# Kernel tuning notes

Hardware: AMD Instinct MI355X
Metric: run time of the kernel (lower is better)

Reference implementation:

```python
import jax, jax.numpy as jnp
import numpy as np

B, T, V, E, H = 512, 256, 50000, 512, 1024


def setup_inputs() -> dict:
    key = jax.random.key(0)
    ks = jax.random.split(key, 10)
    s_in = 1.0 / np.sqrt(E + H)  # torch Linear default init scale
    s_fc = 1.0 / np.sqrt(H)
    return {
        "x": jax.random.randint(ks[0], (B, T), 0, V),
        "emb": jax.random.normal(ks[1], (V, E), dtype=jnp.float32),
        "W_r": jax.random.uniform(ks[2], (E + H, H), jnp.float32, -s_in, s_in),
        "b_r": jax.random.uniform(ks[3], (H,), jnp.float32, -s_in, s_in),
        "W_z": jax.random.uniform(ks[4], (E + H, H), jnp.float32, -s_in, s_in),
        "b_z": jax.random.uniform(ks[5], (H,), jnp.float32, -s_in, s_in),
        "W_c": jax.random.uniform(ks[6], (E + H, H), jnp.float32, -s_in, s_in),
        "b_c": jax.random.uniform(ks[7], (H,), jnp.float32, -s_in, s_in),
        "W_fc": jax.random.uniform(ks[8], (H, 1), jnp.float32, -s_fc, s_fc),
        "b_fc": jax.random.uniform(ks[9], (1,), jnp.float32, -s_fc, s_fc),
    }


def reference(x, emb, W_r, b_r, W_z, b_z, W_c, b_c, W_fc, b_fc):
    embedded = emb[x]                      # [B, T, E]
    xs = jnp.swapaxes(embedded, 0, 1)      # [T, B, E] for scan over time
    h0 = jnp.zeros((x.shape[0], H), dtype=emb.dtype)

    # fuse r and z gates: same input, one GEMM
    W_rz = jnp.concatenate([W_r, W_z], axis=1)   # [E+H, 2H]
    b_rz = jnp.concatenate([b_r, b_z], axis=0)   # [2H]

    def step(h, xt):
        combined = jnp.concatenate([xt, h], axis=1)          # [B, E+H]
        rz = jax.nn.sigmoid(combined @ W_rz + b_rz)          # [B, 2H]
        r, z = rz[:, :H], rz[:, H:]
        cc = jnp.concatenate([xt, r * h], axis=1)            # [B, E+H]
        h_tilde = jnp.tanh(cc @ W_c + b_c)                   # [B, H]
        h_new = (1.0 - z) * h + z * h_tilde
        return h_new, None

    h_T, _ = jax.lax.scan(step, h0, xs)
    return jax.nn.sigmoid(h_T @ W_fc + b_fc)                 # [B, 1]
```

## Files before the change

kernel.cpp:

```cpp
#include <hip/hip_runtime.h>
#include <hip/hip_bf16.h>

#define B_ 512
#define T_ 256
#define E_ 512
#define H_ 1024
#define K_ 1536

typedef __attribute__((ext_vector_type(4))) float f32x4;
typedef __attribute__((ext_vector_type(8))) short s16x8;
typedef __attribute__((ext_vector_type(4))) unsigned int u32x4;
typedef __attribute__((ext_vector_type(2))) unsigned int u32x2;

typedef unsigned int u32_g __attribute__((address_space(1)));
typedef unsigned int u32_l __attribute__((address_space(3)));

static __device__ __forceinline__ void gload16(const void* g, void* l) {
    __builtin_amdgcn_global_load_lds((const u32_g*)g, (u32_l*)l, 16, 0, 0);
}

static __device__ __forceinline__ short f2b(float f) {
    union { float f; unsigned u; } v; v.f = f;
    unsigned r = v.u + 0x7FFFu + ((v.u >> 16) & 1u);
    return (short)(r >> 16);
}
static __device__ __forceinline__ float bf2f(short s) {
    union { unsigned u; float f; } v; v.u = ((unsigned)(unsigned short)s) << 16;
    return v.f;
}
static __device__ __forceinline__ float sigmoidf_(float v) {
    return 1.f / (1.f + expf(-v));
}

#define WAITV(n) asm volatile("s_waitcnt vmcnt(" #n ")" ::: "memory")
#define WAITL    asm volatile("s_waitcnt lgkmcnt(0)" ::: "memory")
#define SB0 __builtin_amdgcn_sched_barrier(0)

static __device__ __forceinline__ u32x4 load16sc(const short* p) {
    u32x4 r;
    asm volatile("global_load_dwordx4 %0, %1, off sc1" : "=v"(r) : "v"(p));
    return r;
}
static __device__ __forceinline__ u32x2 load8sc(const short* p) {
    u32x2 r;
    asm volatile("global_load_dwordx2 %0, %1, off sc1" : "=v"(r) : "v"(p));
    return r;
}
static __device__ __forceinline__ void store2sc(const short* p, unsigned v) {
    asm volatile("global_store_short %0, %1, off sc1" :: "v"(p), "v"(v) : "memory");
}

#define FR(buf, row, k) \
    (*(const s16x8*)&(buf)[(row) * 128 + ((((k) >> 3) ^ ((row) & 7)) << 3)])


__global__ __launch_bounds__(256) void prep_fast(
    const float* __restrict__ W_r, const float* __restrict__ W_z,
    const float* __restrict__ W_c, const float* __restrict__ emb,
    short* __restrict__ We, short* __restrict__ Wh, short* __restrict__ embb,
    float* __restrict__ hbuf, short* __restrict__ hb16, unsigned* __restrict__ flags)
{
    const int NW = 3072 * 1536;
    const int NE = 50048 * 512;
    const int NH = 512 * 1024;
    const int NF = 8192;
    const int total = NW + NE + NH + NF;
    for (int idx = blockIdx.x * 256 + threadIdx.x; idx < total; idx += gridDim.x * 256) {
        if (idx < NW) {
            int n = idx / 1536, k = idx - n * 1536;
            const float* W = n < 1024 ? W_r : (n < 2048 ? W_z : W_c);
            float v = W[(size_t)k * 1024 + (n & 1023)];
            if (k < 512) We[(size_t)n * 512 + k] = f2b(v);
            else         Wh[(size_t)n * 1024 + (k - 512)] = f2b(v);
        } else if (idx < NW + NE) {
            int e = idx - NW; int row = e >> 9;
            embb[e] = row < 50000 ? f2b(emb[e]) : (short)0;
        } else if (idx < NW + NE + NH) {
            int h = idx - NW - NE;
            hbuf[h] = 0.f; hb16[h] = 0;
        } else {
            flags[idx - NW - NE - NH] = 0u;
        }
    }
}

__global__ __launch_bounds__(256) void vproj_gemm(
    const short* __restrict__ embb, const short* __restrict__ We,
    short* __restrict__ vp)
{
    __shared__ short As[128 * 64];
    __shared__ short Bs[128 * 64];
    const int tid = threadIdx.x, lane = tid & 63, w = tid >> 6;
    const int wm = (w >> 1) * 64, wn = (w & 1) * 64;
    const int m0 = blockIdx.x * 128, n0 = blockIdx.y * 128;
    f32x4 acc[4][4] = {};
    for (int kc = 0; kc < 8; ++kc) {
        int k0 = kc * 64;
        #pragma unroll
        for (int ii = 0; ii < 4; ++ii) {
            int i = w * 4 + ii;
            int row = i * 8 + (lane >> 3), kk = (lane & 7) * 8;
            gload16(embb + (size_t)(m0 + row) * 512 + k0 + kk, As + i * 512);
            gload16(We   + (size_t)(n0 + row) * 512 + k0 + kk, Bs + i * 512);
        }
        __syncthreads();
        #pragma unroll
        for (int kk = 0; kk < 64; kk += 32) {
            s16x8 a[4], b[4];
            #pragma unroll
            for (int f = 0; f < 4; ++f) {
                a[f] = *(const s16x8*)&As[(wm + f * 16 + (lane & 15)) * 64 + kk + (lane >> 4) * 8];
                b[f] = *(const s16x8*)&Bs[(wn + f * 16 + (lane & 15)) * 64 + kk + (lane >> 4) * 8];
            }
            #pragma unroll
            for (int fm = 0; fm < 4; ++fm)
            #pragma unroll
            for (int fn = 0; fn < 4; ++fn)
                acc[fm][fn] = __builtin_amdgcn_mfma_f32_16x16x32_bf16(a[fm], b[fn], acc[fm][fn], 0, 0, 0);
        }
        __syncthreads();
    }
    #pragma unroll
    for (int fm = 0; fm < 4; ++fm)
    #pragma unroll
    for (int fn = 0; fn < 4; ++fn)
    #pragma unroll
    for (int r = 0; r < 4; ++r) {
        int row = m0 + wm + fm * 16 + (lane >> 4) * 4 + r;
        int col = n0 + wn + fn * 16 + (lane & 15);
        vp[(size_t)row * 3072 + col] = f2b(acc[fm][fn][r]);
    }
}

static __device__ __forceinline__ void barrier_fs(unsigned* gf, int member, unsigned gen) {
    __builtin_amdgcn_s_barrier();
    if (threadIdx.x == 0)
        __hip_atomic_store(&gf[member * 16], gen,
                           __ATOMIC_RELAXED, __HIP_MEMORY_SCOPE_AGENT);
    if ((threadIdx.x & 63) < 32) {
        int spins = 0;
        while (__hip_atomic_load(&gf[(threadIdx.x & 31) * 16],
                                 __ATOMIC_RELAXED, __HIP_MEMORY_SCOPE_AGENT) < gen) {
            __builtin_amdgcn_s_sleep(1);
            if (++spins > (1 << 18)) break;
        }
    }
    __builtin_amdgcn_s_barrier();
}

static __device__ __forceinline__ void issueA2(const short* Ab, int c, u32x4* dst) {
    const int tid = threadIdx.x;
    #pragma unroll
    for (int j = 0; j < 2; ++j) {
        int sid = j * 256 + tid, row = sid >> 4, sg = (sid & 15) ^ (row & 7);
        dst[j] = load16sc(Ab + (size_t)row * 1024 + c * 128 + sg * 8);
    }
}
static __device__ __forceinline__ void writeA2(short* AL, int buf, const u32x4* src) {
    const int tid = threadIdx.x;
    #pragma unroll
    for (int j = 0; j < 2; ++j) {
        int sid = j * 256 + tid;
        *(u32x4*)&AL[buf * 4096 + sid * 8] = src[j];
    }
}
template<int PH>
static __device__ __forceinline__ void issueB(const short* Wh, short* BL, int n, int c, int buf) {
    const int tid = threadIdx.x, lane = tid & 63, w = tid >> 6;
    constexpr int BJ    = (PH == 1) ? 4 : 2;
    constexpr int BUFSZ = (PH == 1) ? 8192 : 4096;
    #pragma unroll
    for (int j = 0; j < BJ; ++j) {
        int sid = j * 256 + tid, row = sid >> 4, sg = (sid & 15) ^ (row & 7);
        int grow;
        if constexpr (PH == 1) grow = (row < 32) ? (n * 32 + row) : (1024 + n * 32 + row - 32);
        else                   grow = 2048 + n * 32 + row;
        gload16(Wh + (size_t)grow * 1024 + c * 128 + sg * 8,
                BL + buf * BUFSZ + (j * 256 + w * 64) * 8);
    }
}
template<int PH>
static __device__ __forceinline__ u32x4 gather_xp(const short* vp, int xv, int n) {
    const int part = threadIdx.x & 7;
    u32x4 r = {};
    if constexpr (PH == 1) {
        int col = (part < 4) ? (n * 32 + part * 8) : (1024 + n * 32 + (part - 4) * 8);
        r = load16sc(vp + (size_t)xv * 3072 + col);
    } else {
        u32x2 t2 = load8sc(vp + (size_t)xv * 3072 + 2048 + n * 32 + part * 4);
        r.x = t2.x; r.y = t2.y;
    }
    return r;
}

template<int PH>
static __device__ __forceinline__ void phase_run(
    const short* __restrict__ Ab, const short* __restrict__ Wh,
    int g, int n, int t,
    short* AL, short* BL, short* XpL, float* zL, short* hL,
    const float* br, const float* bz, float bc, u32x4 xp,
    short* __restrict__ rh16, short* __restrict__ hb16,
    float* __restrict__ hbuf, f32x4& h_reg)
{
    const int tid = threadIdx.x, lane = tid & 63, w = tid >> 6;
    const int wm = (w >> 1) * 16;
    const int wn = (PH == 1) ? (w & 1) * 32 : (w & 1) * 16;
    constexpr int BUFSZ = (PH == 1) ? 8192 : 4096;

    u32x4 ra[4][2];
    issueA2(Ab, 0, ra[0]); issueA2(Ab, 1, ra[1]);
    issueA2(Ab, 2, ra[2]); issueA2(Ab, 3, ra[3]);
    WAITV(6); SB0;
    writeA2(AL, 0, ra[0]);
    {
        int row = tid >> 3, part = tid & 7;
        if constexpr (PH == 1) {
            int dst = (part < 4) ? part * 8 : (32 + (part - 4) * 8);
            *(u32x4*)&XpL[row * 64 + dst] = xp;
        } else {
            u32x2 v2; v2.x = xp.x; v2.y = xp.y;
            *(u32x2*)&XpL[row * 32 + part * 4] = v2;
        }
    }
    WAITL;
    __builtin_amdgcn_s_barrier();
    SB0;

    f32x4 acc0 = {}, acc1 = {};
    #pragma unroll
    for (int kc = 0; kc < 8; ++kc) {
        if (kc < 4) issueA2(Ab, kc + 4, ra[kc & 3]);
        if (kc < 6) issueB<PH>(Wh, BL, n, kc + 2, (kc + 2) % 3);
        SB0;
        const short* Ac = AL + (kc & 1) * 4096;
        const short* Bc = BL + (kc % 3) * BUFSZ;
        #pragma unroll
        for (int ks = 0; ks < 4; ++ks) {
            const int kf = ks * 32 + (lane >> 4) * 8;
            s16x8 a  = FR(Ac, wm + (lane & 15), kf);
            s16x8 b0 = FR(Bc, wn + (lane & 15), kf);
            acc0 = __builtin_amdgcn_mfma_f32_16x16x32_bf16(a, b0, acc0, 0, 0, 0);
            if constexpr (PH == 1) {
                s16x8 b1 = FR(Bc, wn + 16 + (lane & 15), kf);
                acc1 = __builtin_amdgcn_mfma_f32_16x16x32_bf16(a, b1, acc1, 0, 0, 0);
            }
        }
        if (kc < 7) {
            if constexpr (PH == 1) {
                if (kc == 0) { WAITV(10); } else if (kc <= 3) { WAITV(6); }
                else if (kc <= 5) { WAITV(4); } else { WAITV(0); }
            } else {
                if (kc == 0) { WAITV(8); } else if (kc <= 3) { WAITV(4); }
                else if (kc <= 5) { WAITV(2); } else { WAITV(0); }
            }
            SB0;
            writeA2(AL, (kc + 1) & 1, ra[(kc + 1) & 3]);
            WAITL;
            __builtin_amdgcn_s_barrier();
            SB0;
        } else {
            SB0;
            __builtin_amdgcn_s_barrier();
        }
    }

    const int rl0 = wm + (lane >> 4) * 4;
    if constexpr (PH == 1) {
        if ((w & 1) == 0) {
            #pragma unroll
            for (int fn = 0; fn < 2; ++fn) {
                int cl = fn * 16 + (lane & 15);
                #pragma unroll
                for (int ri = 0; ri < 4; ++ri) {
                    int rl = rl0 + ri;
                    float v = (fn ? acc1[ri] : acc0[ri]) + bf2f(XpL[rl * 64 + cl]) + br[fn];
                    float rr = sigmoidf_(v);
                    float hv = bf2f(hL[rl * 32 + cl]);
                    store2sc(rh16 + (size_t)(g * 32 + rl) * 1024 + n * 32 + cl,
                             (unsigned)(unsigned short)f2b(rr * hv));
                }
            }
        } else {
            #pragma unroll
            for (int fn = 0; fn < 2; ++fn) {
                int zc = fn * 16 + (lane & 15);
                #pragma unroll
                for (int ri = 0; ri < 4; ++ri) {
                    int rl = rl0 + ri;
                    float v = (fn ? acc1[ri] : acc0[ri]) + bf2f(XpL[rl * 64 + 32 + zc]) + bz[fn];
                    zL[rl * 32 + zc] = sigmoidf_(v);
                }
            }
        }
    } else {
        const int cl = wn + (lane & 15);
        #pragma unroll
        for (int ri = 0; ri < 4; ++ri) {
            int rl = rl0 + ri;
            float v = acc0[ri] + bf2f(XpL[rl * 32 + cl]) + bc;
            float c = tanhf(v);
            float zv = zL[rl * 32 + cl];
            float h = h_reg[ri];
            float hn = h + zv * (c - h);
            h_reg[ri] = hn;
            short hb = f2b(hn);
            store2sc(hb16 + (size_t)(g * 32 + rl) * 1024 + n * 32 + cl,
                     (unsigned)(unsigned short)hb);
            hL[rl * 32 + cl] = hb;
            if (t == T_ - 1)
                hbuf[(size_t)(g * 32 + rl) * 1024 + n * 32 + cl] = hn;
        }
    }
}

__global__ __launch_bounds__(256, 2) void gru_persistent(
    const int* __restrict__ x, const short* __restrict__ Wh,
    const short* __restrict__ vp,
    const float* __restrict__ b_r, const float* __restrict__ b_z,
    const float* __restrict__ b_c,
    float* __restrict__ hbuf, short* __restrict__ hb16,
    short* __restrict__ rh16, unsigned* __restrict__ flags)
{
    __shared__ short AL[2 * 4096];
    __shared__ short BL[3 * 8192];
    __shared__ short XpL[2048];
    __shared__ float zL[1024];
    __shared__ short hL[1024];

    const int bid = blockIdx.x;
    const int g = bid >> 5, n = bid & 31;
    unsigned* gf = flags + g * 512;
    const int tid = threadIdx.x, lane = tid & 63, w = tid >> 6;

    float br[2], bz[2];
    #pragma unroll
    for (int fn = 0; fn < 2; ++fn) {
        br[fn] = b_r[n * 32 + fn * 16 + (lane & 15)];
        bz[fn] = b_z[n * 32 + fn * 16 + (lane & 15)];
    }
    const float bc = b_c[n * 32 + (w & 1) * 16 + (lane & 15)];

    f32x4 h_reg = {0.f, 0.f, 0.f, 0.f};
    ((u32x2*)hL)[tid] = (u32x2){0u, 0u};

    const short* Ab1 = hb16 + (size_t)(g * 32) * 1024;
    const short* Ab2 = rh16 + (size_t)(g * 32) * 1024;

    int xv = x[(g * 32 + (tid >> 3)) * T_ + 0];
    SB0;
    u32x4 xp = gather_xp<1>(vp, xv, n);
    issueB<1>(Wh, BL, n, 0, 0);
    issueB<1>(Wh, BL, n, 1, 1);
    SB0;

    for (int t = 0; t < T_; ++t) {
        phase_run<1>(Ab1, Wh, g, n, t, AL, BL, XpL, zL, hL,
                     br, bz, bc, xp, rh16, hb16, hbuf, h_reg);
        u32x4 xp2 = gather_xp<2>(vp, xv, n);
        issueB<2>(Wh, BL, n, 0, 0);
        issueB<2>(Wh, BL, n, 1, 1);
        WAITV(5);
        WAITL;
        SB0;
        barrier_fs(gf, n, 2 * t + 1);

        int xv_next = x[(g * 32 + (tid >> 3)) * T_ + ((t < T_ - 1) ? t + 1 : t)];
        SB0;
        phase_run<2>(Ab2, Wh, g, n, t, AL, BL, XpL, zL, hL,
                     br, bz, bc, xp2, rh16, hb16, hbuf, h_reg);
        xv = xv_next;
        xp = gather_xp<1>(vp, xv, n);
        issueB<1>(Wh, BL, n, 0, 0);
        issueB<1>(Wh, BL, n, 1, 1);
        WAITV(9);
        WAITL;
        SB0;
        if (t < T_ - 1) barrier_fs(gf, n, 2 * t + 2);
    }
}

__global__ __launch_bounds__(256) void fc_kernel(
    const float* __restrict__ h, const float* __restrict__ Wfc,
    const float* __restrict__ bfc, float* __restrict__ out)
{
    int gw   = (blockIdx.x * 256 + threadIdx.x) >> 6;
    int lane = threadIdx.x & 63;
    if (gw >= B_) return;
    float s = 0.f;
    for (int j = lane; j < H_; j += 64) s += h[(size_t)gw * H_ + j] * Wfc[j];
    #pragma unroll
    for (int off = 32; off; off >>= 1) s += __shfl_down(s, off);
    if (lane == 0) out[gw] = sigmoidf_(s + bfc[0]);
}

__global__ __launch_bounds__(256) void prep_fb(
    const float* __restrict__ W_r, const float* __restrict__ W_z,
    const float* __restrict__ W_c,
    short* __restrict__ Wt_rz, short* __restrict__ Wt_c,
    float* __restrict__ hbuf, short* __restrict__ hbf16)
{
    const int PER = H_ * K_;
    int idx = blockIdx.x * 256 + threadIdx.x;
    if (idx < PER * 3) {
        int mm = idx / PER, rem = idx - mm * PER;
        int n = rem / K_, k = rem - n * K_;
        if (mm == 0)      Wt_rz[(size_t)n * K_ + k]        = f2b(W_r[(size_t)k * H_ + n]);
        else if (mm == 1) Wt_rz[(size_t)(H_ + n) * K_ + k] = f2b(W_z[(size_t)k * H_ + n]);
        else              Wt_c[(size_t)n * K_ + k]         = f2b(W_c[(size_t)k * H_ + n]);
    }
    if (idx < B_ * H_) { hbuf[idx] = 0.f; hbf16[idx] = 0; }
}

template<int MODE>
__global__ __launch_bounds__(256) void gru_gemm(
    const int* __restrict__ x, const float* __restrict__ emb,
    const short* __restrict__ Wt, const short* __restrict__ hpart,
    const float* __restrict__ bias0, const float* __restrict__ bias1,
    const float* __restrict__ hbuf, float* __restrict__ zbuf,
    short* __restrict__ rh_out, float* __restrict__ h_out,
    short* __restrict__ hb_out, int t)
{
    __shared__ short As2[64][72];
    __shared__ short Bs2[64][72];
    __shared__ int xidx2[64];
    const int tid = threadIdx.x;
    const int bm = blockIdx.x, bn = blockIdx.y;
    if (tid < 64) xidx2[tid] = x[(bm * 64 + tid) * T_ + t];
    f32x4 acc[2][2] = {};
    const int m  = tid >> 2;
    const int ks = (tid & 3) * 16;
    const int w  = tid >> 6, lane = tid & 63;
    const int wm = (w >> 1) * 32, wn = (w & 1) * 32;
    const int lr = lane & 15, lk = (lane >> 4) * 8;
    __syncthreads();
    for (int kt = 0; kt < 24; ++kt) {
        const int k0 = kt * 64;
        if (k0 < E_) {
            const int row = xidx2[m];
            const float4* src = (const float4*)&emb[(size_t)row * E_ + k0 + ks];
            short tmp[16];
            #pragma unroll
            for (int v = 0; v < 4; ++v) {
                float4 f = src[v];
                tmp[v*4+0] = f2b(f.x); tmp[v*4+1] = f2b(f.y);
                tmp[v*4+2] = f2b(f.z); tmp[v*4+3] = f2b(f.w);
            }
            *(s16x8*)&As2[m][ks]     = *(const s16x8*)&tmp[0];
            *(s16x8*)&As2[m][ks + 8] = *(const s16x8*)&tmp[8];
        } else {
            const s16x8* src = (const s16x8*)&hpart[(size_t)(bm*64 + m) * H_ + (k0 - E_ + ks)];
            *(s16x8*)&As2[m][ks]     = src[0];
            *(s16x8*)&As2[m][ks + 8] = src[1];
        }
        {
            const s16x8* src = (const s16x8*)&Wt[(size_t)(bn*64 + m) * K_ + k0 + ks];
            *(s16x8*)&Bs2[m][ks]     = src[0];
            *(s16x8*)&Bs2[m][ks + 8] = src[1];
        }
        __syncthreads();
        #pragma unroll
        for (int kk = 0; kk < 64; kk += 32) {
            s16x8 a0 = *(const s16x8*)&As2[wm      + lr][kk + lk];
            s16x8 a1 = *(const s16x8*)&As2[wm + 16 + lr][kk + lk];
            s16x8 b0 = *(const s16x8*)&Bs2[wn      + lr][kk + lk];
            s16x8 b1 = *(const s16x8*)&Bs2[wn + 16 + lr][kk + lk];
            acc[0][0] = __builtin_amdgcn_mfma_f32_16x16x32_bf16(a0, b0, acc[0][0], 0, 0, 0);
            acc[0][1] = __builtin_amdgcn_mfma_f32_16x16x32_bf16(a0, b1, acc[0][1], 0, 0, 0);
            acc[1][0] = __builtin_amdgcn_mfma_f32_16x16x32_bf16(a1, b0, acc[1][0], 0, 0, 0);
            acc[1][1] = __builtin_amdgcn_mfma_f32_16x16x32_bf16(a1, b1, acc[1][1], 0, 0, 0);
        }
        __syncthreads();
    }
    #pragma unroll
    for (int fm = 0; fm < 2; ++fm)
    #pragma unroll
    for (int fn = 0; fn < 2; ++fn)
    #pragma unroll
    for (int r = 0; r < 4; ++r) {
        const int row = bm * 64 + wm + fm * 16 + ((lane >> 4) * 4 + r);
        const int n   = bn * 64 + wn + fn * 16 + (lane & 15);
        float v = acc[fm][fn][r];
        if (MODE == 0) {
            if (n < H_) {
                float rr = sigmoidf_(v + bias0[n]);
                size_t idx = (size_t)row * H_ + n;
                rh_out[idx] = f2b(rr * hbuf[idx]);
            } else {
                int nz = n - H_;
                zbuf[(size_t)row * H_ + nz] = sigmoidf_(v + bias1[nz]);
            }
        } else {
            float ht = tanhf(v + bias0[n]);
            size_t idx = (size_t)row * H_ + n;
            float h = hbuf[idx], z = zbuf[idx];
            float hn = (1.f - z) * h + z * ht;
            h_out[idx]  = hn;
            hb_out[idx] = f2b(hn);
        }
    }
}

extern "C" void kernel_launch(void* const* d_in, const int* in_sizes, int n_in,
                              void* d_out, int out_size, void* d_ws, size_t ws_size,
                              hipStream_t stream) {
    const int*   x    = (const int*)  d_in[0];
    const float* emb  = (const float*)d_in[1];
    const float* W_r  = (const float*)d_in[2];
    const float* b_r  = (const float*)d_in[3];
    const float* W_z  = (const float*)d_in[4];
    const float* b_z  = (const float*)d_in[5];
    const float* W_c  = (const float*)d_in[6];
    const float* b_c  = (const float*)d_in[7];
    const float* W_fc = (const float*)d_in[8];
    const float* b_fc = (const float*)d_in[9];

    char* ws = (char*)d_ws;
    const size_t NEED = 374489088ULL;

    if (ws_size >= NEED) {
        short*    We    = (short*)(ws);
        short*    Wh    = (short*)(ws + 3145728);
        short*    embb  = (short*)(ws + 9437184);
        short*    vp    = (short*)(ws + 60686336);
        float*    hbuf  = (float*)(ws + 368181248);
        short*    hb16  = (short*)(ws + 370278400);
        short*    rh16  = (short*)(ws + 371326976);
        unsigned* flags = (unsigned*)(ws + 372375552);

        prep_fast<<<2048, 256, 0, stream>>>(W_r, W_z, W_c, emb, We, Wh, embb, hbuf, hb16, flags);
        vproj_gemm<<<dim3(391, 24), 256, 0, stream>>>(embb, We, vp);
        gru_persistent<<<512, 256, 0, stream>>>(x, Wh, vp, b_r, b_z, b_c,
                                                hbuf, hb16, rh16, flags);
        fc_kernel<<<128, 256, 0, stream>>>(hbuf, W_fc, b_fc, (float*)d_out);
    } else {
        short* Wt_rz  = (short*)(ws);
        short* Wt_c   = (short*)(ws + 6291456);
        float* hbuf   = (float*)(ws + 9437184);
        short* hbf16  = (short*)(ws + 11534336);
        short* rhbf16 = (short*)(ws + 12582912);
        float* zbuf   = (float*)(ws + 13631488);

        prep_fb<<<18432, 256, 0, stream>>>(W_r, W_z, W_c, Wt_rz, Wt_c, hbuf, hbf16);
        for (int t = 0; t < T_; ++t) {
            gru_gemm<0><<<dim3(8, 32), 256, 0, stream>>>(
                x, emb, Wt_rz, hbf16, b_r, b_z, hbuf, zbuf, rhbf16, nullptr, nullptr, t);
            gru_gemm<1><<<dim3(8, 16), 256, 0, stream>>>(
                x, emb, Wt_c, rhbf16, b_c, nullptr, hbuf, zbuf, nullptr, hbuf, hbf16, t);
        }
        fc_kernel<<<128, 256, 0, stream>>>(hbuf, W_fc, b_fc, (float*)d_out);
    }
}
```

Baseline: 5.999 ms.

## Load MFMA operands directly from global into registers, bypassing LDS staging

The persistent GRU step kernel stops staging the hidden-state A tiles and weight B tiles through shared memory. Each wave now loads its own MFMA fragments straight from global memory into registers, using a 4-slot A ring and a 3-slot B ring with hand-counted vmcnt waits. This removes the per-chunk LDS writes and workgroup barriers, and weights are read without the sc1 cache hint. The cost is much higher register pressure and redundant global reads of B fragments across waves. The cross-phase weight prefetch before the grid barrier is also dropped, so weight loads are no longer overlapped with the barrier wait.

```diff
diff --git a/kernel.cpp b/kernel.cpp
--- a/kernel.cpp
+++ b/kernel.cpp
@@ -41,6 +41,11 @@
     asm volatile("global_load_dwordx4 %0, %1, off sc1" : "=v"(r) : "v"(p));
     return r;
 }
+static __device__ __forceinline__ u32x4 load16l2(const short* p) {
+    u32x4 r;
+    asm volatile("global_load_dwordx4 %0, %1, off" : "=v"(r) : "v"(p));
+    return r;
+}
 static __device__ __forceinline__ u32x2 load8sc(const short* p) {
     u32x2 r;
     asm volatile("global_load_dwordx2 %0, %1, off sc1" : "=v"(r) : "v"(p));
@@ -49,9 +54,6 @@
 static __device__ __forceinline__ void store2sc(const short* p, unsigned v) {
     asm volatile("global_store_short %0, %1, off sc1" :: "v"(p), "v"(v) : "memory");
 }
-
-#define FR(buf, row, k) \
-    (*(const s16x8*)&(buf)[(row) * 128 + ((((k) >> 3) ^ ((row) & 7)) << 3)])
 
 
 __global__ __launch_bounds__(256) void prep_fast(
@@ -148,37 +150,6 @@
     __builtin_amdgcn_s_barrier();
 }
 
-static __device__ __forceinline__ void issueA2(const short* Ab, int c, u32x4* dst) {
-    const int tid = threadIdx.x;
-    #pragma unroll
-    for (int j = 0; j < 2; ++j) {
-        int sid = j * 256 + tid, row = sid >> 4, sg = (sid & 15) ^ (row & 7);
-        dst[j] = load16sc(Ab + (size_t)row * 1024 + c * 128 + sg * 8);
-    }
-}
-static __device__ __forceinline__ void writeA2(short* AL, int buf, const u32x4* src) {
-    const int tid = threadIdx.x;
-    #pragma unroll
-    for (int j = 0; j < 2; ++j) {
-        int sid = j * 256 + tid;
-        *(u32x4*)&AL[buf * 4096 + sid * 8] = src[j];
-    }
-}
-template<int PH>
-static __device__ __forceinline__ void issueB(const short* Wh, short* BL, int n, int c, int buf) {
-    const int tid = threadIdx.x, lane = tid & 63, w = tid >> 6;
-    constexpr int BJ    = (PH == 1) ? 4 : 2;
-    constexpr int BUFSZ = (PH == 1) ? 8192 : 4096;
-    #pragma unroll
-    for (int j = 0; j < BJ; ++j) {
-        int sid = j * 256 + tid, row = sid >> 4, sg = (sid & 15) ^ (row & 7);
-        int grow;
-        if constexpr (PH == 1) grow = (row < 32) ? (n * 32 + row) : (1024 + n * 32 + row - 32);
-        else                   grow = 2048 + n * 32 + row;
-        gload16(Wh + (size_t)grow * 1024 + c * 128 + sg * 8,
-                BL + buf * BUFSZ + (j * 256 + w * 64) * 8);
-    }
-}
 template<int PH>
 static __device__ __forceinline__ u32x4 gather_xp(const short* vp, int xv, int n) {
     const int part = threadIdx.x & 7;
@@ -194,24 +165,42 @@
 }
 
 template<int PH>
-static __device__ __forceinline__ void phase_run(
+static __device__ __forceinline__ void phase_runR(
     const short* __restrict__ Ab, const short* __restrict__ Wh,
     int g, int n, int t,
-    short* AL, short* BL, short* XpL, float* zL, short* hL,
+    short* XpL, float* zL, short* hL,
     const float* br, const float* bz, float bc, u32x4 xp,
     short* __restrict__ rh16, short* __restrict__ hb16,
     float* __restrict__ hbuf, f32x4& h_reg)
 {
     const int tid = threadIdx.x, lane = tid & 63, w = tid >> 6;
     const int wm = (w >> 1) * 16;
-    const int wn = (PH == 1) ? (w & 1) * 32 : (w & 1) * 16;
-    constexpr int BUFSZ = (PH == 1) ? 8192 : 4096;
-
-    u32x4 ra[4][2];
-    issueA2(Ab, 0, ra[0]); issueA2(Ab, 1, ra[1]);
-    issueA2(Ab, 2, ra[2]); issueA2(Ab, 3, ra[3]);
-    WAITV(6); SB0;
-    writeA2(AL, 0, ra[0]);
+    const int kof = (lane >> 4) * 8;
+    const short* Abase = Ab + (size_t)(wm + (lane & 15)) * 1024 + kof;
+    int brow0;
+    if constexpr (PH == 1) brow0 = ((w & 1) ? 1024 : 0) + n * 32 + (lane & 15);
+    else                   brow0 = 2048 + n * 32 + (w & 1) * 16 + (lane & 15);
+    const short* Bbase = Wh + (size_t)brow0 * 1024 + kof;
+    constexpr int CT = (PH == 1) ? 2 : 1;
+
+    u32x4 fa[4][4];
+    u32x4 fb[3][CT][4];
+
+#define ISSA(slot, c) { _Pragma("unroll") for (int ks = 0; ks < 4; ++ks) \
+    fa[slot][ks] = load16sc(Abase + (c) * 128 + ks * 32); }
+#define ISSB(slot, c) { _Pragma("unroll") for (int ct = 0; ct < CT; ++ct) \
+    { _Pragma("unroll") for (int ks = 0; ks < 4; ++ks) \
+      fb[slot][ct][ks] = load16l2(Bbase + (size_t)ct * 16384 + (c) * 128 + ks * 32); } }
+#define MF(as, bs) { _Pragma("unroll") for (int ks = 0; ks < 4; ++ks) { \
+    s16x8 a_ = *(s16x8*)&fa[as][ks]; \
+    acc0 = __builtin_amdgcn_mfma_f32_16x16x32_bf16(a_, *(s16x8*)&fb[bs][0][ks], acc0, 0, 0, 0); \
+    if constexpr (PH == 1) \
+        acc1 = __builtin_amdgcn_mfma_f32_16x16x32_bf16(a_, *(s16x8*)&fb[bs][CT-1][ks], acc1, 0, 0, 0); } }
+
+    ISSA(0, 0) ISSA(1, 1) ISSA(2, 2)
+    ISSB(0, 0) ISSB(1, 1)
+    if constexpr (PH == 1) { WAITV(28); } else { WAITV(20); }
+    SB0;
     {
         int row = tid >> 3, part = tid & 7;
         if constexpr (PH == 1) {
@@ -227,42 +216,24 @@
     SB0;
 
     f32x4 acc0 = {}, acc1 = {};
-    #pragma unroll
-    for (int kc = 0; kc < 8; ++kc) {
-        if (kc < 4) issueA2(Ab, kc + 4, ra[kc & 3]);
-        if (kc < 6) issueB<PH>(Wh, BL, n, kc + 2, (kc + 2) % 3);
-        SB0;
-        const short* Ac = AL + (kc & 1) * 4096;
-        const short* Bc = BL + (kc % 3) * BUFSZ;
-        #pragma unroll
-        for (int ks = 0; ks < 4; ++ks) {
-            const int kf = ks * 32 + (lane >> 4) * 8;
-            s16x8 a  = FR(Ac, wm + (lane & 15), kf);
-            s16x8 b0 = FR(Bc, wn + (lane & 15), kf);
-            acc0 = __builtin_amdgcn_mfma_f32_16x16x32_bf16(a, b0, acc0, 0, 0, 0);
-            if constexpr (PH == 1) {
-                s16x8 b1 = FR(Bc, wn + 16 + (lane & 15), kf);
-                acc1 = __builtin_amdgcn_mfma_f32_16x16x32_bf16(a, b1, acc1, 0, 0, 0);
-            }
-        }
-        if (kc < 7) {
-            if constexpr (PH == 1) {
-                if (kc == 0) { WAITV(10); } else if (kc <= 3) { WAITV(6); }
-                else if (kc <= 5) { WAITV(4); } else { WAITV(0); }
-            } else {
-                if (kc == 0) { WAITV(8); } else if (kc <= 3) { WAITV(4); }
-                else if (kc <= 5) { WAITV(2); } else { WAITV(0); }
-            }
-            SB0;
-            writeA2(AL, (kc + 1) & 1, ra[(kc + 1) & 3]);
-            WAITL;
-            __builtin_amdgcn_s_barrier();
-            SB0;
-        } else {
-            SB0;
-            __builtin_amdgcn_s_barrier();
-        }
-    }
+    ISSA(3, 3) ISSB(2, 2)
+    if constexpr (PH == 1) { WAITV(20); } else { WAITV(12); }  SB0;  MF(0, 0)
+    ISSA(0, 4) ISSB(0, 3)
+    if constexpr (PH == 1) { WAITV(24); } else { WAITV(16); }  SB0;  MF(1, 1)
+    ISSA(1, 5) ISSB(1, 4)
+    if constexpr (PH == 1) { WAITV(24); } else { WAITV(16); }  SB0;  MF(2, 2)
+    ISSA(2, 6) ISSB(2, 5)
+    if constexpr (PH == 1) { WAITV(24); } else { WAITV(16); }  SB0;  MF(3, 0)
+    ISSA(3, 7) ISSB(0, 6)
+    if constexpr (PH == 1) { WAITV(24); } else { WAITV(16); }  SB0;  MF(0, 1)
+    ISSB(1, 7)
+    if constexpr (PH == 1) { WAITV(20); } else { WAITV(12); }  SB0;  MF(1, 2)
+    if constexpr (PH == 1) { WAITV(8);  } else { WAITV(4);  }  SB0;  MF(2, 0)
+    WAITV(0);                                                  SB0;  MF(3, 1)
+
+#undef ISSA
+#undef ISSB
+#undef MF
 
     const int rl0 = wm + (lane >> 4) * 4;
     if constexpr (PH == 1) {
@@ -293,7 +264,7 @@
             }
         }
     } else {
-        const int cl = wn + (lane & 15);
+        const int cl = (w & 1) * 16 + (lane & 15);
         #pragma unroll
         for (int ri = 0; ri < 4; ++ri) {
             int rl = rl0 + ri;
@@ -321,8 +292,6 @@
     float* __restrict__ hbuf, short* __restrict__ hb16,
     short* __restrict__ rh16, unsigned* __restrict__ flags)
 {
-    __shared__ short AL[2 * 4096];
-    __shared__ short BL[3 * 8192];
     __shared__ short XpL[2048];
     __shared__ float zL[1024];
     __shared__ short hL[1024];
@@ -349,30 +318,24 @@
     int xv = x[(g * 32 + (tid >> 3)) * T_ + 0];
     SB0;
     u32x4 xp = gather_xp<1>(vp, xv, n);
-    issueB<1>(Wh, BL, n, 0, 0);
-    issueB<1>(Wh, BL, n, 1, 1);
     SB0;
 
     for (int t = 0; t < T_; ++t) {
-        phase_run<1>(Ab1, Wh, g, n, t, AL, BL, XpL, zL, hL,
-                     br, bz, bc, xp, rh16, hb16, hbuf, h_reg);
+        phase_runR<1>(Ab1, Wh, g, n, t, XpL, zL, hL,
+                      br, bz, bc, xp, rh16, hb16, hbuf, h_reg);
         u32x4 xp2 = gather_xp<2>(vp, xv, n);
-        issueB<2>(Wh, BL, n, 0, 0);
-        issueB<2>(Wh, BL, n, 1, 1);
-        WAITV(5);
+        WAITV(1);
         WAITL;
         SB0;
         barrier_fs(gf, n, 2 * t + 1);
 
         int xv_next = x[(g * 32 + (tid >> 3)) * T_ + ((t < T_ - 1) ? t + 1 : t)];
         SB0;
-        phase_run<2>(Ab2, Wh, g, n, t, AL, BL, XpL, zL, hL,
-                     br, bz, bc, xp2, rh16, hb16, hbuf, h_reg);
+        phase_runR<2>(Ab2, Wh, g, n, t, XpL, zL, hL,
+                      br, bz, bc, xp2, rh16, hb16, hbuf, h_reg);
         xv = xv_next;
         xp = gather_xp<1>(vp, xv, n);
-        issueB<1>(Wh, BL, n, 0, 0);
-        issueB<1>(Wh, BL, n, 1, 1);
-        WAITV(9);
+        WAITV(1);
         WAITL;
         SB0;
         if (t < T_ - 1) barrier_fs(gf, n, 2 * t + 2);
```

Result: slower. 16.97 ms (+182.9%).
